# Kernel optimization log

Hardware: AMD Instinct MI355X
Metric: run time of the kernel (lower is better)

Reference implementation:

```python
import jax, jax.numpy as jnp
import numpy as np

BIN_AGG = 16  # binAgg in source
K = 3         # forward-default im2col/col2im kernel size


def _im2col(x, k):
    # torch Im2Col (unfold), pad=0, stride=1, dilation=1
    B, C, H, W = x.shape
    oh, ow = H - k + 1, W - k + 1
    patches = [x[:, :, i:i + oh, j:j + ow] for i in range(k) for j in range(k)]
    cols = jnp.stack(patches, axis=2)            # [B, C, k*k, oh, ow]
    return cols.reshape(B, C * k * k, oh * ow)   # [B, C*k*k, L]


def _col2im(cols, k, H, W):
    # torch Col2Im (fold): overlap-add of patches back to [B, C, H, W]
    B, CK, L = cols.shape
    C = CK // (k * k)
    oh = H - k + 1
    cols = cols.reshape(B, C, k, k, oh, oh)
    img = jnp.zeros((B, C, H, W), cols.dtype)
    for i in range(k):
        for j in range(k):
            img = img.at[:, :, i:i + oh, j:j + oh].add(cols[:, :, i, j])
    return img


def bin_active(x):
    # sign(x) scaled by block-wise mean of |x| over blocks of 16 along last dim
    B, Kd, L = x.shape
    blocks = jnp.abs(x).reshape(B, Kd, L // BIN_AGG, BIN_AGG)
    scale = jnp.mean(blocks, axis=-1, keepdims=True)
    scale = jnp.broadcast_to(scale, blocks.shape).reshape(B, Kd, L)
    return scale * jnp.sign(x)


def setup_inputs() -> dict:
    key = jax.random.key(0)
    ks = jax.random.split(key, 5)
    B, Cin, Cout, H = 8, 64, 128, 130
    x = jax.random.normal(ks[0], (B, Cin, H, H), jnp.float32)
    gamma = 1.0 + 0.1 * jax.random.normal(ks[1], (Cin,), jnp.float32)
    beta = 0.1 * jax.random.normal(ks[2], (Cin,), jnp.float32)
    conv_w = 0.05 * jax.random.normal(ks[3], (Cout, Cin, 3, 3), jnp.float32)
    conv_b = 0.05 * jax.random.normal(ks[4], (Cout,), jnp.float32)
    return {"x": x, "gamma": gamma, "beta": beta, "conv_w": conv_w, "conv_b": conv_b}


def reference(x, gamma, beta, conv_w, conv_b):
    eps = 1e-4  # BatchNorm2d eps in source
    # BatchNorm2d (training-mode batch statistics, affine)
    mean = jnp.mean(x, axis=(0, 2, 3), keepdims=True)
    var = jnp.var(x, axis=(0, 2, 3), keepdims=True)
    xbn = (x - mean) * jax.lax.rsqrt(var + eps) * gamma[None, :, None, None] + beta[None, :, None, None]
    H = x.shape[2]
    cols = _im2col(xbn, K)          # [B, C*9, (H-2)^2]
    cols = bin_active(cols)         # block-mean binary quantization
    img = _col2im(cols, K, H, H)    # [B, C, H, W]
    y = jax.lax.conv_general_dilated(
        img, conv_w, window_strides=(1, 1), padding=((1, 1), (1, 1)),
        dimension_numbers=("NCHW", "OIHW", "NCHW"))
    y = y + conv_b[None, :, None, None]
    return jax.nn.relu(y)
```

## Files before the change

### kernel.cpp

```cpp
#include <hip/hip_runtime.h>
#include <math.h>

#define B_    8
#define CIN   64
#define COUT  128
#define H_    130
#define NPIX  (H_*H_)
#define NPX   (B_*NPIX)
#define IMW   132
#define ROWE  (8*IMW*8)

typedef __attribute__((ext_vector_type(8))) short short8;
typedef __attribute__((ext_vector_type(4))) float f32x4;

__device__ __forceinline__ ushort f2bf(float f) {
    uint u = __builtin_bit_cast(uint, f);
    uint r = (u + 0x7FFFu + ((u >> 16) & 1u)) >> 16;
    return (ushort)r;
}

__global__ __launch_bounds__(256) void bn_stage1(
    const float* __restrict__ x, float* __restrict__ part)
{
    const int c = blockIdx.x, b = blockIdx.y, tid = threadIdx.x;
    const float4* p = (const float4*)(x + ((size_t)b*CIN + c)*NPIX);
    float s = 0.f, q = 0.f;
    for (int i = tid; i < NPIX/4; i += 256) {
        float4 v = p[i];
        s += v.x + v.y + v.z + v.w;
        q += v.x*v.x + v.y*v.y + v.z*v.z + v.w*v.w;
    }
    #pragma unroll
    for (int off = 32; off; off >>= 1) { s += __shfl_down(s, off); q += __shfl_down(q, off); }
    __shared__ float ss[4], qq[4];
    if ((tid & 63) == 0) { ss[tid >> 6] = s; qq[tid >> 6] = q; }
    __syncthreads();
    if (tid == 0) {
        s = ss[0] + ss[1] + ss[2] + ss[3];
        q = qq[0] + qq[1] + qq[2] + qq[3];
        part[(c*B_ + b)*2]     = s;
        part[(c*B_ + b)*2 + 1] = q;
    }
}

__global__ __launch_bounds__(256) void wprep_bn(
    const float* __restrict__ w, const float* __restrict__ part,
    const float* __restrict__ gamma, const float* __restrict__ beta,
    ushort* __restrict__ wT, float* __restrict__ abuf, float* __restrict__ bbuf)
{
    int i = blockIdx.x*256 + threadIdx.x;
    int co = i / 576, k = i - co*576;
    int dydx = k >> 6, ci = k & 63;
    wT[i] = f2bf(w[co*576 + ci*9 + dydx]);
    if (blockIdx.x == 0 && threadIdx.x < 64) {
        int c = threadIdx.x;
        float s = 0.f, q = 0.f;
        for (int b = 0; b < B_; ++b) { s += part[(c*B_+b)*2]; q += part[(c*B_+b)*2+1]; }
        float mean = s * (1.0f/135200.f);
        float var  = q * (1.0f/135200.f) - mean*mean;
        float a = gamma[c] / sqrtf(var + 1e-4f);
        abuf[c] = a;
        bbuf[c] = beta[c] - mean * a;
    }
}

__global__ __launch_bounds__(256) void binfold(
    const float* __restrict__ x, const float* __restrict__ abuf,
    const float* __restrict__ bbuf, ushort* __restrict__ img)
{
    __shared__ __align__(16) ushort tile[H_*18];
    __shared__ float absrow[4][132];
    __shared__ float wsum[4][24];
    const int yy = blockIdx.x, b = blockIdx.y, zg = blockIdx.z;
    const int tid = threadIdx.x, wv = tid >> 6, lane = tid & 63;
    uint* rowU = (uint*)(img + (size_t)(b*IMW + yy)*ROWE);
    const int cgBase = zg*2;

    if (yy == 0 || yy == IMW-1) {
        for (int i = tid; i < 2*IMW*4; i += 256)
            rowU[cgBase*IMW*4 + i] = 0u;
        return;
    }
    const int y = yy - 1;
    const float county = (float)min(min(y + 1, 3), H_ - y);

    const int ci0 = zg*16 + wv*4;
    float v0[4], v1[4], v2[4];
    #pragma unroll
    for (int it = 0; it < 4; ++it) {
        const int ci = ci0 + it;
        const float* row = x + (((size_t)b*CIN + ci)*H_ + y)*H_;
        const float a = abuf[ci], bb = bbuf[ci];
        v0[it] = a*row[lane]      + bb;
        v1[it] = a*row[lane + 64] + bb;
        v2[it] = (lane < 2) ? (a*row[lane + 128] + bb) : 0.f;
    }

    #pragma unroll
    for (int it = 0; it < 4; ++it) {
        const int cl = wv*4 + it;
        absrow[wv][lane]      = fabsf(v0[it]);
        absrow[wv][lane + 64] = fabsf(v1[it]);
        if (lane < 2) absrow[wv][lane + 128] = fabsf(v2[it]);
        asm volatile("s_waitcnt lgkmcnt(0)" ::: "memory");
        if (lane < 24) {
            int j = lane >> 3, bx = lane & 7;
            int s = j + bx*16;
            float acc = 0.f;
            #pragma unroll
            for (int t = 0; t < 16; ++t) acc += absrow[wv][s + t];
            wsum[wv][j*8 + bx] = acc;
        }
        asm volatile("s_waitcnt lgkmcnt(0)" ::: "memory");
        #pragma unroll
        for (int rep = 0; rep < 3; ++rep) {
            int xp = lane + rep*64;
            if (xp < H_) {
                float v = (rep == 0) ? v0[it] : (rep == 1) ? v1[it] : v2[it];
                float sgn = (v > 0.f) ? 1.f : ((v < 0.f) ? -1.f : 0.f);
                float sum = 0.f;
                #pragma unroll
                for (int j = 0; j < 3; ++j) {
                    int ox = xp - j;
                    if ((unsigned)ox < 128u) sum += wsum[wv][j*8 + (ox >> 4)];
                }
                tile[xp*18 + cl] = f2bf(sgn * county * sum * 0.0625f);
            }
        }
        asm volatile("s_waitcnt lgkmcnt(0)" ::: "memory");
    }
    __syncthreads();
    const uint* tU = (const uint*)tile;
    for (int i = tid; i < H_*8; i += 256) {
        int xp = i >> 3, p = i & 7;
        rowU[((cgBase + (p >> 2))*IMW + xp + 1)*4 + (p & 3)] = tU[xp*9 + p];
    }
    if (tid < 16) {
        int cg = cgBase + (tid >> 3), side = (tid >> 2) & 1, u = tid & 3;
        rowU[(cg*IMW + (side ? (IMW-1) : 0))*4 + u] = 0u;
    }
}

__global__ __launch_bounds__(256, 3) void conv_mfma(
    const ushort* __restrict__ img, const ushort* __restrict__ wT,
    const float* __restrict__ bias, float* __restrict__ out)
{
    __shared__ __align__(16) ushort sB[3*ROWE];
    const int y = blockIdx.x, b = blockIdx.y;
    const int tid = threadIdx.x, lane = tid & 63, wv = tid >> 6;
    const int l16 = lane & 15, quad = lane >> 4;
    const int mh = wv >> 1, nh = wv & 1;

    {
        const uint4* src = (const uint4*)(img + (size_t)(b*IMW + y)*ROWE);
        uint4* dst = (uint4*)sB;
        for (int i = tid; i < 3*ROWE/8; i += 256) dst[i] = src[i];
    }
    __syncthreads();

    int xBase[5];
    #pragma unroll
    for (int nt = 0; nt < 5; ++nt)
        xBase[nt] = min(nh*80 + nt*16 + l16, 129);

    const ushort* wA = wT + (size_t)(mh*64 + l16)*576 + quad*8;
    const int bQuad = quad*132;

    f32x4 acc[4][5];
    #pragma unroll
    for (int mt = 0; mt < 4; ++mt)
        #pragma unroll
        for (int nt = 0; nt < 5; ++nt)
            acc[mt][nt] = (f32x4){0.f, 0.f, 0.f, 0.f};

    short8 aCur[4];
    #pragma unroll
    for (int mt = 0; mt < 4; ++mt)
        aCur[mt] = *(const short8*)(wA + mt*16*576);

    #pragma unroll
    for (int s = 0; s < 18; ++s) {
        short8 aNxt[4];
        if (s < 17) {
            #pragma unroll
            for (int mt = 0; mt < 4; ++mt)
                aNxt[mt] = *(const short8*)(wA + mt*16*576 + (s+1)*32);
        }
        const int dydx = s >> 1, h = s & 1;
        const int dy = dydx / 3, dx = dydx - dy*3;
        const int gOff = ((dy*8 + h*4)*132 + dx)*8;
        short8 bf[5];
        #pragma unroll
        for (int nt = 0; nt < 5; ++nt)
            bf[nt] = *(const short8*)(sB + gOff + (bQuad + xBase[nt])*8);
        #pragma unroll
        for (int mt = 0; mt < 4; ++mt)
            #pragma unroll
            for (int nt = 0; nt < 5; ++nt)
                acc[mt][nt] = __builtin_amdgcn_mfma_f32_16x16x32_bf16(
                    aCur[mt], bf[nt], acc[mt][nt], 0, 0, 0);
        #pragma unroll
        for (int mt = 0; mt < 4; ++mt) aCur[mt] = aNxt[mt];
    }

    const size_t ob = (size_t)b*COUT*NPIX + (size_t)y*H_;
    #pragma unroll
    for (int mt = 0; mt < 4; ++mt) {
        #pragma unroll
        for (int r = 0; r < 4; ++r) {
            const int co = mh*64 + mt*16 + quad*4 + r;
            const float bv = bias[co];
            #pragma unroll
            for (int nt = 0; nt < 5; ++nt) {
                int p = nh*80 + nt*16 + l16;
                if (p < H_) {
                    float v = acc[mt][nt][r] + bv;
                    out[ob + (size_t)co*NPIX + p] = v > 0.f ? v : 0.f;
                }
            }
        }
    }
}

extern "C" void kernel_launch(void* const* d_in, const int* in_sizes, int n_in,
                              void* d_out, int out_size, void* d_ws, size_t ws_size,
                              hipStream_t stream)
{
    const float* x      = (const float*)d_in[0];
    const float* gamma  = (const float*)d_in[1];
    const float* beta   = (const float*)d_in[2];
    const float* conv_w = (const float*)d_in[3];
    const float* conv_b = (const float*)d_in[4];
    float* out = (float*)d_out;

    float*  part = (float*)d_ws;
    float*  abuf = part + 1024;
    float*  bbuf = abuf + 64;
    ushort* wT   = (ushort*)(bbuf + 64);
    ushort* img  = wT + 73728;

    bn_stage1<<<dim3(CIN, B_), 256, 0, stream>>>(x, part);
    wprep_bn<<<288, 256, 0, stream>>>(conv_w, part, gamma, beta, wT, abuf, bbuf);
    binfold<<<dim3(IMW, B_, 4), 256, 0, stream>>>(x, abuf, bbuf, img);
    conv_mfma<<<dim3(H_, B_), 256, 0, stream>>>(img, wT, conv_b, out);
}
```

Baseline: 192.2 us.

## Split conv rows into half-width slabs with direct global-to-LDS loads

Changes the intermediate image layout to two half-row slabs of 72 columns, 65 of them valid plus halo, so each conv block handles half a row. Each wave now covers 32 output channels across the full half-row instead of a 2x2 M/N split. The tile is staged with global_load_lds instead of register copies. Weight fragments are prefetched two steps ahead, and the occupancy hint rises to 4 blocks per CU. The grid doubles and the accumulator count per thread halves, trading more blocks and some halo reload for higher occupancy and less LDS per block.

```diff
diff --git a/kernel.cpp b/kernel.cpp
--- a/kernel.cpp
+++ b/kernel.cpp
@@ -8,7 +8,7 @@
 #define NPIX  (H_*H_)
 #define NPX   (B_*NPIX)
 #define IMW   132
-#define ROWE  (8*IMW*8)
+#define SLABU 4608
 
 typedef __attribute__((ext_vector_type(8))) short short8;
 typedef __attribute__((ext_vector_type(4))) float f32x4;
@@ -73,12 +73,14 @@
     __shared__ float wsum[4][24];
     const int yy = blockIdx.x, b = blockIdx.y, zg = blockIdx.z;
     const int tid = threadIdx.x, wv = tid >> 6, lane = tid & 63;
-    uint* rowU = (uint*)(img + (size_t)(b*IMW + yy)*ROWE);
     const int cgBase = zg*2;
+    uint* u0 = (uint*)(img + ((size_t)(b*IMW + yy)*2)*SLABU);
 
     if (yy == 0 || yy == IMW-1) {
-        for (int i = tid; i < 2*IMW*4; i += 256)
-            rowU[cgBase*IMW*4 + i] = 0u;
+        for (int i = tid; i < 1088; i += 256) {
+            int xhh = i / 544, r = i - xhh*544, c = r >> 3, p = r & 7;
+            u0[(size_t)xhh*(SLABU/2) + ((cgBase + (p>>2))*72 + c)*4 + (p&3)] = 0u;
+        }
         return;
     }
     const int y = yy - 1;
@@ -131,89 +133,94 @@
     }
     __syncthreads();
     const uint* tU = (const uint*)tile;
-    for (int i = tid; i < H_*8; i += 256) {
-        int xp = i >> 3, p = i & 7;
-        rowU[((cgBase + (p >> 2))*IMW + xp + 1)*4 + (p & 3)] = tU[xp*9 + p];
-    }
-    if (tid < 16) {
-        int cg = cgBase + (tid >> 3), side = (tid >> 2) & 1, u = tid & 3;
-        rowU[(cg*IMW + (side ? (IMW-1) : 0))*4 + u] = 0u;
-    }
-}
-
-__global__ __launch_bounds__(256, 3) void conv_mfma(
+    for (int i = tid; i < 1088; i += 256) {
+        int xhh = i / 544, r = i - xhh*544, c = r >> 3, p = r & 7;
+        int xx = xhh*65 + c;
+        if (xx > 131) continue;
+        uint v = 0u;
+        if (xx != 0 && xx != 131) v = tU[(xx-1)*9 + p];
+        u0[(size_t)xhh*(SLABU/2) + ((cgBase + (p>>2))*72 + c)*4 + (p&3)] = v;
+    }
+}
+
+__global__ __launch_bounds__(256, 4) void conv_mfma(
     const ushort* __restrict__ img, const ushort* __restrict__ wT,
     const float* __restrict__ bias, float* __restrict__ out)
 {
-    __shared__ __align__(16) ushort sB[3*ROWE];
-    const int y = blockIdx.x, b = blockIdx.y;
-    const int tid = threadIdx.x, lane = tid & 63, wv = tid >> 6;
+    __shared__ __align__(64) ushort sB[3*SLABU];
+    const int xh = blockIdx.x, y = blockIdx.y, b = blockIdx.z;
+    const int tid = threadIdx.x, lane = tid & 63, q = tid >> 6;
     const int l16 = lane & 15, quad = lane >> 4;
-    const int mh = wv >> 1, nh = wv & 1;
 
     {
-        const uint4* src = (const uint4*)(img + (size_t)(b*IMW + y)*ROWE);
-        uint4* dst = (uint4*)sB;
-        for (int i = tid; i < 3*ROWE/8; i += 256) dst[i] = src[i];
+        const size_t rowBase = ((size_t)(b*IMW + y)*2 + xh);
+        #pragma unroll
+        for (int t = 0; t < 7; ++t) {
+            int k = q + 4*t;
+            if (k < 27) {
+                int dy = (int)((unsigned)k / 9u), j = k - dy*9;
+                const ushort* gs = img + (rowBase + (size_t)dy*2)*SLABU + j*512 + lane*8;
+                ushort* ls = sB + k*512;
+                __builtin_amdgcn_global_load_lds(
+                    (const __attribute__((address_space(1))) uint*)gs,
+                    (__attribute__((address_space(3))) uint*)ls, 16, 0, 0);
+            }
+        }
     }
     __syncthreads();
 
-    int xBase[5];
+    const ushort* wA = wT + (size_t)(q*32 + l16)*576 + quad*8;
+    short8 aP[3][2];
+    #pragma unroll
+    for (int mt = 0; mt < 2; ++mt) {
+        aP[0][mt] = *(const short8*)(wA + mt*16*576);
+        aP[1][mt] = *(const short8*)(wA + mt*16*576 + 32);
+    }
+    int colB[5];
     #pragma unroll
     for (int nt = 0; nt < 5; ++nt)
-        xBase[nt] = min(nh*80 + nt*16 + l16, 129);
-
-    const ushort* wA = wT + (size_t)(mh*64 + l16)*576 + quad*8;
-    const int bQuad = quad*132;
-
-    f32x4 acc[4][5];
-    #pragma unroll
-    for (int mt = 0; mt < 4; ++mt)
+        colB[nt] = min(nt*16 + l16, 64);
+
+    f32x4 acc[2][5];
+    #pragma unroll
+    for (int mt = 0; mt < 2; ++mt)
         #pragma unroll
         for (int nt = 0; nt < 5; ++nt)
             acc[mt][nt] = (f32x4){0.f, 0.f, 0.f, 0.f};
 
-    short8 aCur[4];
-    #pragma unroll
-    for (int mt = 0; mt < 4; ++mt)
-        aCur[mt] = *(const short8*)(wA + mt*16*576);
-
     #pragma unroll
     for (int s = 0; s < 18; ++s) {
-        short8 aNxt[4];
-        if (s < 17) {
-            #pragma unroll
-            for (int mt = 0; mt < 4; ++mt)
-                aNxt[mt] = *(const short8*)(wA + mt*16*576 + (s+1)*32);
+        if (s < 16) {
+            #pragma unroll
+            for (int mt = 0; mt < 2; ++mt)
+                aP[(s+2)%3][mt] = *(const short8*)(wA + mt*16*576 + (s+2)*32);
         }
         const int dydx = s >> 1, h = s & 1;
         const int dy = dydx / 3, dx = dydx - dy*3;
-        const int gOff = ((dy*8 + h*4)*132 + dx)*8;
+        const int base = dy*SLABU + ((h*4 + quad)*72 + dx)*8;
         short8 bf[5];
         #pragma unroll
         for (int nt = 0; nt < 5; ++nt)
-            bf[nt] = *(const short8*)(sB + gOff + (bQuad + xBase[nt])*8);
-        #pragma unroll
-        for (int mt = 0; mt < 4; ++mt)
+            bf[nt] = *(const short8*)(sB + base + colB[nt]*8);
+        #pragma unroll
+        for (int mt = 0; mt < 2; ++mt)
             #pragma unroll
             for (int nt = 0; nt < 5; ++nt)
                 acc[mt][nt] = __builtin_amdgcn_mfma_f32_16x16x32_bf16(
-                    aCur[mt], bf[nt], acc[mt][nt], 0, 0, 0);
-        #pragma unroll
-        for (int mt = 0; mt < 4; ++mt) aCur[mt] = aNxt[mt];
-    }
-
-    const size_t ob = (size_t)b*COUT*NPIX + (size_t)y*H_;
-    #pragma unroll
-    for (int mt = 0; mt < 4; ++mt) {
+                    aP[s%3][mt], bf[nt], acc[mt][nt], 0, 0, 0);
+    }
+
+    const size_t ob = (size_t)b*COUT*NPIX + (size_t)y*H_ + xh*65;
+    #pragma unroll
+    for (int mt = 0; mt < 2; ++mt) {
         #pragma unroll
         for (int r = 0; r < 4; ++r) {
-            const int co = mh*64 + mt*16 + quad*4 + r;
+            const int co = q*32 + mt*16 + quad*4 + r;
             const float bv = bias[co];
             #pragma unroll
             for (int nt = 0; nt < 5; ++nt) {
-                int p = nh*80 + nt*16 + l16;
-                if (p < H_) {
+                int p = nt*16 + l16;
+                if (p < 65) {
                     float v = acc[mt][nt][r] + bv;
                     out[ob + (size_t)co*NPIX + p] = v > 0.f ? v : 0.f;
                 }
@@ -242,5 +249,5 @@
     bn_stage1<<<dim3(CIN, B_), 256, 0, stream>>>(x, part);
     wprep_bn<<<288, 256, 0, stream>>>(conv_w, part, gamma, beta, wT, abuf, bbuf);
     binfold<<<dim3(IMW, B_, 4), 256, 0, stream>>>(x, abuf, bbuf, img);
-    conv_mfma<<<dim3(H_, B_), 256, 0, stream>>>(img, wT, conv_b, out);
-}
+    conv_mfma<<<dim3(2, H_, B_), 256, 0, stream>>>(img, wT, conv_b, out);
+}
```

Measured after the change: 185.6 us. 3.5% less time.
